# Kernel tuning notes

Hardware: AMD Instinct MI355X
Metric: run time of the kernel (lower is better)

Reference implementation:

```python
import jax, jax.numpy as jnp
import numpy as np

KERNEL = 3
PAD = (KERNEL - 1) // 2
KA = KERNEL * KERNEL          # kernel_area = 9
CENTER = KA // 2              # 4
CH_OUT = 64


def setup_inputs() -> dict:
    key = jax.random.key(0)
    k1, k2 = jax.random.split(key)
    x = jax.random.normal(k1, (8, 64, 128, 128), dtype=jnp.float32)
    weight = jax.random.uniform(k2, (1, 1, KA, 1, 1), dtype=jnp.float32)
    bias = jnp.zeros((1, 1, KA, 1, 1), dtype=jnp.float32)
    weight_center = jnp.ones((), dtype=jnp.float32)
    weight_median = jnp.ones((), dtype=jnp.float32)
    return {"x": x, "weight": weight, "bias": bias,
            "weight_center": weight_center, "weight_median": weight_median}


def _unfold_same(x):
    # x: (B, C, H, W) -> patches (B, C, KA, H, W), stride 1, zero pad
    B, C, H, W = x.shape
    xp = jnp.pad(x, ((0, 0), (0, 0), (PAD, PAD), (PAD, PAD)))
    # order matches F.unfold: index = ki*K + kj
    views = [xp[:, :, i:i + H, j:j + W] for i in range(KERNEL) for j in range(KERNEL)]
    return jnp.stack(views, axis=2)


def reference(x, weight, bias, weight_center, weight_median):
    B, C, H, W = x.shape
    x_sig = jax.nn.sigmoid(x)
    patches = _unfold_same(x_sig)                      # (B, C, KA, H, W)
    w = jax.nn.sigmoid(weight)
    b = jax.nn.sigmoid(bias)
    D = jnp.maximum(w, patches) + b                    # (B, C, KA, H, W)
    max_stat = jnp.sum(D, axis=2)
    # torch.median returns the lower middle element -> sort and index (KA-1)//2
    median_stat = jnp.sort(D, axis=2)[:, :, (KA - 1) // 2]
    mean_stat = jnp.mean(D, axis=2)
    center = patches[:, :, CENTER]
    out = (weight_center * center + weight_median * median_stat
           - max_stat - mean_stat)                     # (B, C, H, W)
    # expand to ch_out then sum over C_in -> every output channel is identical
    s = jnp.sum(out, axis=1)                           # (B, H, W)
    return jnp.broadcast_to(s[:, None], (B, CH_OUT, H, W))
```

## Files before the change

kernel.cpp:

```cpp
#include <hip/hip_runtime.h>

#define BATCH  8
#define CH     64
#define H      128
#define W      128
#define TH     4
#define CHUNK  8
#define NCHUNK (CH / CHUNK)
#define HWID   (W + 2)
#define HHGT   (TH + 2)
#define HALO_N (HWID * HHGT)
#define NSLOT  4

__device__ __forceinline__ float sigmoidf_(float v) {
    return 1.0f / (1.0f + __expf(-v));
}

__global__ __launch_bounds__(256) void partial_kernel(
    const float* __restrict__ x,
    const float* __restrict__ weight,
    const float* __restrict__ bias,
    const float* __restrict__ wcp,
    const float* __restrict__ wmp,
    float* __restrict__ out)
{
    __shared__ float sm[HALO_N];

    const int tid  = threadIdx.x;
    const int tx   = tid & (W - 1);
    const int ty0  = (tid >> 7) * 2;
    const int by   = blockIdx.x;
    const int chnk = blockIdx.y;
    const int b    = blockIdx.z;

    bool has[NSLOT], ok[NSLOT];
    int  off[NSLOT];
    #pragma unroll
    for (int s = 0; s < NSLOT; ++s) {
        int i  = tid + s * 256;
        has[s] = (i < HALO_N);
        int ic = has[s] ? i : (HALO_N - 1);
        int yy = ic / HWID;
        int xx = ic - yy * HWID;
        int sy = by * TH + yy - 1;
        int sx = xx - 1;
        ok[s]  = (sy >= 0 && sy < H && sx >= 0 && sx < W);
        off[s] = min(max(sy, 0), H - 1) * W + min(max(sx, 0), W - 1);
    }

    float wk[9], bk[9];
    #pragma unroll
    for (int k = 0; k < 9; ++k) {
        wk[k] = sigmoidf_(weight[k]);
        bk[k] = sigmoidf_(bias[k]);
    }
    const float wc = wcp[0];
    const float wm = wmp[0];

    const float* xb = x + ((size_t)b * CH + chnk * CHUNK) * H * W;

    float r[NSLOT];
    #pragma unroll
    for (int s = 0; s < NSLOT; ++s) r[s] = xb[off[s]];

    float acc0 = 0.0f, acc1 = 0.0f;

    for (int c = 0; c < CHUNK; ++c) {
        #pragma unroll
        for (int s = 0; s < NSLOT; ++s)
            if (has[s]) sm[tid + s * 256] = ok[s] ? sigmoidf_(r[s]) : 0.0f;
        __syncthreads();

        if (c + 1 < CHUNK) {
            const float* xn = xb + (size_t)(c + 1) * H * W;
            #pragma unroll
            for (int s = 0; s < NSLOT; ++s) r[s] = xn[off[s]];
        }

        float v[4][3];
        #pragma unroll
        for (int dy = 0; dy < 4; ++dy)
            #pragma unroll
            for (int dx = 0; dx < 3; ++dx)
                v[dy][dx] = sm[(ty0 + dy) * HWID + tx + dx];

        #pragma unroll
        for (int j = 0; j < 2; ++j) {
            float d[9];
            float sum = 0.0f;
            #pragma unroll
            for (int dy = 0; dy < 3; ++dy)
                #pragma unroll
                for (int dx = 0; dx < 3; ++dx) {
                    int k = dy * 3 + dx;
                    float dk = fmaxf(wk[k], v[j + dy][dx]) + bk[k];
                    d[k] = dk;
                    sum += dk;
                }
            const float center = v[j + 1][1];

            #define S2(a,bb) { float t = d[a]; d[a] = fminf(d[a], d[bb]); d[bb] = fmaxf(t, d[bb]); }
            S2(0,3) S2(1,4) S2(2,5) S2(0,1) S2(0,2) S2(4,5) S2(3,5)
            S2(1,2) S2(3,4) S2(1,3) S2(1,6) S2(4,6) S2(2,6)
            S2(2,3) S2(4,7) S2(2,4) S2(3,7)
            S2(4,8) S2(3,8) S2(3,4)
            #undef S2
            const float med = d[4];

            const float r_ = wc * center + wm * med - sum - sum * (1.0f / 9.0f);
            if (j == 0) acc0 += r_; else acc1 += r_;
        }

        __syncthreads();
    }

    float* op = out + ((size_t)b * CH + chnk) * H * W
                    + (size_t)(by * TH + ty0) * W + tx;
    op[0] = acc0;
    op[W] = acc1;
}

__global__ __launch_bounds__(256) void broadcast_kernel(float* __restrict__ out)
{
    const int g = blockIdx.x * 256 + threadIdx.x;
    const int b = g >> 14;
    const int p = g & 16383;
    float* base = out + (size_t)b * CH * H * W;

    float s = 0.0f;
    #pragma unroll
    for (int k = 0; k < NCHUNK; ++k)
        s += base[(size_t)k * H * W + p];

    #pragma unroll
    for (int co = 0; co < CH; ++co)
        base[(size_t)co * H * W + p] = s;
}

extern "C" void kernel_launch(void* const* d_in, const int* in_sizes, int n_in,
                              void* d_out, int out_size, void* d_ws, size_t ws_size,
                              hipStream_t stream) {
    const float* x      = (const float*)d_in[0];
    const float* weight = (const float*)d_in[1];
    const float* bias   = (const float*)d_in[2];
    const float* wcp    = (const float*)d_in[3];
    const float* wmp    = (const float*)d_in[4];
    float* out = (float*)d_out;

    dim3 grid1(H / TH, NCHUNK, BATCH);
    partial_kernel<<<grid1, 256, 0, stream>>>(x, weight, bias, wcp, wmp, out);

    const int npix = BATCH * H * W;
    broadcast_kernel<<<npix / 256, 256, 0, stream>>>(out);
}
```

Before: 113.7 us.

## Double-buffer halo tile and vectorize broadcast with workspace and nontemporal stores

Double-buffers the shared-memory halo so the next channel's sigmoid tile is written while the current one is consumed, removing one barrier per channel iteration. Partial sums now go to a separate workspace instead of the output buffer. The broadcast kernel uses float4 loads and nontemporal float4 stores and spreads the 64 output channels across a second grid dimension for more parallelism. The costs are twice the LDS per block and a dependence on the workspace being large enough.

Measured after the change: 115.3 us. About the same (+1.4%).

```diff
diff --git a/kernel.cpp b/kernel.cpp
--- a/kernel.cpp
+++ b/kernel.cpp
@@ -11,6 +11,9 @@
 #define HHGT   (TH + 2)
 #define HALO_N (HWID * HHGT)
 #define NSLOT  4
+#define HW     (H * W)
+
+typedef float vfloat4 __attribute__((ext_vector_type(4)));
 
 __device__ __forceinline__ float sigmoidf_(float v) {
     return 1.0f / (1.0f + __expf(-v));
@@ -22,9 +25,9 @@
     const float* __restrict__ bias,
     const float* __restrict__ wcp,
     const float* __restrict__ wmp,
-    float* __restrict__ out)
+    float* __restrict__ ws)
 {
-    __shared__ float sm[HALO_N];
+    __shared__ float sm[2][HALO_N];
 
     const int tid  = threadIdx.x;
     const int tx   = tid & (W - 1);
@@ -57,22 +60,23 @@
     const float wc = wcp[0];
     const float wm = wmp[0];
 
-    const float* xb = x + ((size_t)b * CH + chnk * CHUNK) * H * W;
+    const float* xb = x + ((size_t)b * CH + chnk * CHUNK) * HW;
 
     float r[NSLOT];
     #pragma unroll
     for (int s = 0; s < NSLOT; ++s) r[s] = xb[off[s]];
+    #pragma unroll
+    for (int s = 0; s < NSLOT; ++s)
+        if (has[s]) sm[0][tid + s * 256] = ok[s] ? sigmoidf_(r[s]) : 0.0f;
+    __syncthreads();
 
     float acc0 = 0.0f, acc1 = 0.0f;
 
     for (int c = 0; c < CHUNK; ++c) {
-        #pragma unroll
-        for (int s = 0; s < NSLOT; ++s)
-            if (has[s]) sm[tid + s * 256] = ok[s] ? sigmoidf_(r[s]) : 0.0f;
-        __syncthreads();
+        const int cur = c & 1;
 
         if (c + 1 < CHUNK) {
-            const float* xn = xb + (size_t)(c + 1) * H * W;
+            const float* xn = xb + (size_t)(c + 1) * HW;
             #pragma unroll
             for (int s = 0; s < NSLOT; ++s) r[s] = xn[off[s]];
         }
@@ -82,7 +86,7 @@
         for (int dy = 0; dy < 4; ++dy)
             #pragma unroll
             for (int dx = 0; dx < 3; ++dx)
-                v[dy][dx] = sm[(ty0 + dy) * HWID + tx + dx];
+                v[dy][dx] = sm[cur][(ty0 + dy) * HWID + tx + dx];
 
         #pragma unroll
         for (int j = 0; j < 2; ++j) {
@@ -111,30 +115,41 @@
             if (j == 0) acc0 += r_; else acc1 += r_;
         }
 
+        if (c + 1 < CHUNK) {
+            #pragma unroll
+            for (int s = 0; s < NSLOT; ++s)
+                if (has[s]) sm[cur ^ 1][tid + s * 256] = ok[s] ? sigmoidf_(r[s]) : 0.0f;
+        }
         __syncthreads();
     }
 
-    float* op = out + ((size_t)b * CH + chnk) * H * W
-                    + (size_t)(by * TH + ty0) * W + tx;
+    float* op = ws + ((size_t)b * NCHUNK + chnk) * HW
+                   + (size_t)(by * TH + ty0) * W + tx;
     op[0] = acc0;
     op[W] = acc1;
 }
 
-__global__ __launch_bounds__(256) void broadcast_kernel(float* __restrict__ out)
+__global__ __launch_bounds__(256) void broadcast_kernel(
+    const float* __restrict__ ws,
+    float* __restrict__ out)
 {
-    const int g = blockIdx.x * 256 + threadIdx.x;
-    const int b = g >> 14;
-    const int p = g & 16383;
-    float* base = out + (size_t)b * CH * H * W;
+    const int g  = (blockIdx.x * 256 + threadIdx.x) * 4;
+    const int b  = g >> 14;
+    const int p  = g & (HW - 1);
+    const int c0 = blockIdx.y * 16;
 
-    float s = 0.0f;
+    const float* wsb = ws + (size_t)b * NCHUNK * HW + p;
+    vfloat4 s = (vfloat4)(0.0f);
     #pragma unroll
-    for (int k = 0; k < NCHUNK; ++k)
-        s += base[(size_t)k * H * W + p];
+    for (int k = 0; k < NCHUNK; ++k) {
+        vfloat4 v = *(const vfloat4*)(wsb + (size_t)k * HW);
+        s += v;
+    }
 
+    float* base = out + ((size_t)b * CH + c0) * HW + p;
     #pragma unroll
-    for (int co = 0; co < CH; ++co)
-        base[(size_t)co * H * W + p] = s;
+    for (int j = 0; j < 16; ++j)
+        __builtin_nontemporal_store(s, (vfloat4*)(base + (size_t)j * HW));
 }
 
 extern "C" void kernel_launch(void* const* d_in, const int* in_sizes, int n_in,
@@ -146,10 +161,11 @@
     const float* wcp    = (const float*)d_in[3];
     const float* wmp    = (const float*)d_in[4];
     float* out = (float*)d_out;
+    float* ws  = (float*)d_ws;
 
     dim3 grid1(H / TH, NCHUNK, BATCH);
-    partial_kernel<<<grid1, 256, 0, stream>>>(x, weight, bias, wcp, wmp, out);
+    partial_kernel<<<grid1, 256, 0, stream>>>(x, weight, bias, wcp, wmp, ws);
 
-    const int npix = BATCH * H * W;
-    broadcast_kernel<<<npix / 256, 256, 0, stream>>>(out);
+    dim3 grid2(BATCH * HW / (4 * 256), CH / 16);
+    broadcast_kernel<<<grid2, 256, 0, stream>>>(ws, out);
 }
```
